# Optimization experiments

Hardware: AMD Instinct MI355X
Metric: run time of the kernel (lower is better)

## Reference

```python
import jax, jax.numpy as jnp
import numpy as np

SEQ = 512
D_MODEL = 256
NUM_HEADS = 8


def setup_inputs() -> dict:
    key = jax.random.key(0)
    k1, k2, k3, k4, k5, k6 = jax.random.split(key, 6)
    d = D_MODEL
    scale = 1.0 / np.sqrt(d)
    q = jax.random.normal(k1, (SEQ, d), dtype=jnp.float32)
    k = jax.random.normal(k2, (SEQ, d), dtype=jnp.float32)
    v = jax.random.normal(k3, (SEQ, d), dtype=jnp.float32)
    # eqx.nn.Linear weights have shape [out_features, in_features]
    Wq = jax.random.normal(k4, (d, d), dtype=jnp.float32) * scale
    Wk_hyper = jax.random.normal(k5, (d * d, d), dtype=jnp.float32) * scale
    Wv_hyper = jax.random.normal(k6, (d * d, d), dtype=jnp.float32) * scale
    # causal mask: every query row attends to >=1 key, matching softmax(where=mask)
    mask = jnp.tril(jnp.ones((SEQ, SEQ), dtype=bool))
    return {"q": q, "k": k, "v": v, "Wq": Wq, "Wk_hyper": Wk_hyper,
            "Wv_hyper": Wv_hyper, "mask": mask}


def reference(q, k, v, Wq, Wk_hyper, Wv_hyper, mask):
    s, d = q.shape
    n = NUM_HEADS
    dh = d // n
    # q projection (Linear, no bias): y = x @ W.T
    qp = q @ Wq.T                                   # [s, d]
    # hypernetwork per-query projection matrices P[i, j_out, k_in]
    Pk = (qp @ Wk_hyper.T).reshape(s, d, d)         # [s, d, d]
    Pv = (qp @ Wv_hyper.T).reshape(s, d, d)
    # per-query K/V cubes: K[i, l, j] = sum_k Pk[i, j, k] * k[l, k]
    Kc = jnp.einsum('sjk,lk->slj', Pk, k)           # [s, s, d]
    Vc = jnp.einsum('sjk,lk->slj', Pv, v)           # [s, s, d]
    # split heads
    qh = qp.reshape(s, n, dh)                       # [s, n, dh]
    Kh = Kc.reshape(s, s, n, dh)                    # [s_q, s_kv, n, dh]
    Vh = Vc.reshape(s, s, n, dh)
    # NOTE: original scales by 1/sqrt(kv_seq) (k.shape[0]), not sqrt(head_dim)
    logits = jnp.einsum('snd,stnd->nst', qh, Kh) / jnp.sqrt(jnp.float32(s))
    logits = jnp.where(mask[None, :, :], logits, -jnp.inf)
    probs = jax.nn.softmax(logits, axis=-1)         # [n, s_q, s_kv]
    out = jnp.einsum('nst,stnd->snd', probs, Vh)    # [s, n, dh]
    return out.reshape(s, d)
```

## Files before the change

### kernel.cpp

```cpp
#include <hip/hip_runtime.h>
#include <hip/hip_bf16.h>
#include <math.h>

#define SEQ 512
#define DM  256
#define NH  8
#define DH  32
#define DD  (DM*DM)

typedef __attribute__((ext_vector_type(4))) float  f32x4;
typedef __attribute__((ext_vector_type(8))) __bf16 bf16x8;
typedef __attribute__((ext_vector_type(8))) short  s16x8;
typedef __attribute__((ext_vector_type(4))) short  s16x4;

__device__ __forceinline__ unsigned short f2bf(float f) {
  unsigned int u = __builtin_bit_cast(unsigned int, f);
  u += 0x7fffu + ((u >> 16) & 1u);
  return (unsigned short)(u >> 16);
}
__device__ __forceinline__ float bf2f(unsigned short h) {
  unsigned int u = ((unsigned int)h) << 16;
  return __builtin_bit_cast(float, u);
}

__global__ __launch_bounds__(256) void k0_convert(const float* __restrict__ kin,
                                                  const float* __restrict__ vin,
                                                  unsigned short* __restrict__ kbf,
                                                  unsigned short* __restrict__ vT) {
  __shared__ unsigned short tl[64][72];
  int b = blockIdx.x, t = threadIdx.x;
  if (b < 32) {
    int base = b * 4096 + t * 16;
    float4 a0 = *(const float4*)(kin + base);
    float4 a1 = *(const float4*)(kin + base + 4);
    float4 a2 = *(const float4*)(kin + base + 8);
    float4 a3 = *(const float4*)(kin + base + 12);
    s16x8 o0, o1;
    o0[0]=f2bf(a0.x); o0[1]=f2bf(a0.y); o0[2]=f2bf(a0.z); o0[3]=f2bf(a0.w);
    o0[4]=f2bf(a1.x); o0[5]=f2bf(a1.y); o0[6]=f2bf(a1.z); o0[7]=f2bf(a1.w);
    o1[0]=f2bf(a2.x); o1[1]=f2bf(a2.y); o1[2]=f2bf(a2.z); o1[3]=f2bf(a2.w);
    o1[4]=f2bf(a3.x); o1[5]=f2bf(a3.y); o1[6]=f2bf(a3.z); o1[7]=f2bf(a3.w);
    *(s16x8*)(kbf + base)     = o0;
    *(s16x8*)(kbf + base + 8) = o1;
  } else {
    int tb = b - 32;
    int i0 = (tb >> 2) * 64;
    int m0 = (tb & 3) * 64;
    int r = t >> 2, cq = t & 3;
    #pragma unroll
    for (int u = 0; u < 4; u++) {
      float4 x = *(const float4*)(vin + (size_t)(i0 + r) * DM + m0 + cq * 16 + u * 4);
      tl[cq*16 + u*4 + 0][r] = f2bf(x.x);
      tl[cq*16 + u*4 + 1][r] = f2bf(x.y);
      tl[cq*16 + u*4 + 2][r] = f2bf(x.z);
      tl[cq*16 + u*4 + 3][r] = f2bf(x.w);
    }
    __syncthreads();
    int mm = t >> 2;
    s16x8 w0, w1;
    #pragma unroll
    for (int e = 0; e < 8; e++) { w0[e] = tl[mm][cq*16 + e]; w1[e] = tl[mm][cq*16 + 8 + e]; }
    *(s16x8*)(vT + (size_t)(m0 + mm) * SEQ + i0 + cq * 16)     = w0;
    *(s16x8*)(vT + (size_t)(m0 + mm) * SEQ + i0 + cq * 16 + 8) = w1;
  }
}

__global__ __launch_bounds__(256) void k1_qproj(const float* __restrict__ q,
                                                const float* __restrict__ Wq,
                                                float* __restrict__ qpf,
                                                unsigned short* __restrict__ qpb) {
  __shared__ __align__(16) float qrow[DM];
  int i = blockIdx.x, t = threadIdx.x;
  if (t < 64) *(float4*)&qrow[t*4] = *(const float4*)(q + (size_t)i * DM + t * 4);
  __syncthreads();
  int w = t >> 6, lane = t & 63;
  for (int jj = 0; jj < 64; jj++) {
    int j = w * 64 + jj;
    float4 wv = *(const float4*)(Wq + (size_t)j * DM + lane * 4);
    float s = wv.x*qrow[lane*4] + wv.y*qrow[lane*4+1] + wv.z*qrow[lane*4+2] + wv.w*qrow[lane*4+3];
    #pragma unroll
    for (int off = 32; off; off >>= 1) s += __shfl_xor(s, off);
    if (lane == 0) { qpf[(size_t)i*DM + j] = s; qpb[(size_t)i*DM + j] = f2bf(s); }
  }
}

template<int CONVB, int OUTBF>
__global__ __launch_bounds__(256) void gemm_nt(const unsigned short* __restrict__ A,
                                               const void* __restrict__ Bp,
                                               void* __restrict__ Cp,
                                               int M, int N, int K, int nMtiles) {
  __shared__ __align__(16) unsigned short lA[128 * 72];
  __shared__ __align__(16) unsigned short lB[128 * 72];
  int bid = blockIdx.x;
  int mtile = bid % nMtiles, ntile = bid / nMtiles;
  int m0 = mtile * 128, n0 = ntile * 128;
  int t = threadIdx.x;
  int w = t >> 6, lane = t & 63;
  int wr = w >> 1, wc = w & 1;
  f32x4 acc[4][4];
  #pragma unroll
  for (int a = 0; a < 4; a++)
    #pragma unroll
    for (int b = 0; b < 4; b++) acc[a][b] = (f32x4){0.f, 0.f, 0.f, 0.f};

  for (int kt = 0; kt < K; kt += 64) {
    __syncthreads();
    #pragma unroll
    for (int rep = 0; rep < 4; rep++) {
      int sc = rep * 256 + t;
      int row = sc >> 3, c8 = sc & 7;
      *(s16x8*)&lA[row*72 + c8*8] = *(const s16x8*)(A + (size_t)(m0+row)*K + kt + c8*8);
    }
    if (CONVB) {
      const float* B = (const float*)Bp;
      #pragma unroll
      for (int rep = 0; rep < 4; rep++) {
        int sc = rep * 256 + t;
        int row = sc >> 3, c8 = sc & 7;
        const float* src = B + (size_t)(n0+row)*K + kt + c8*8;
        float4 u0 = *(const float4*)src;
        float4 u1 = *(const float4*)(src + 4);
        s16x8 o;
        o[0]=f2bf(u0.x); o[1]=f2bf(u0.y); o[2]=f2bf(u0.z); o[3]=f2bf(u0.w);
        o[4]=f2bf(u1.x); o[5]=f2bf(u1.y); o[6]=f2bf(u1.z); o[7]=f2bf(u1.w);
        *(s16x8*)&lB[row*72 + c8*8] = o;
      }
    } else {
      const unsigned short* B = (const unsigned short*)Bp;
      #pragma unroll
      for (int rep = 0; rep < 4; rep++) {
        int sc = rep * 256 + t;
        int row = sc >> 3, c8 = sc & 7;
        *(s16x8*)&lB[row*72 + c8*8] = *(const s16x8*)(B + (size_t)(n0+row)*K + kt + c8*8);
      }
    }
    __syncthreads();
    #pragma unroll
    for (int kk = 0; kk < 2; kk++) {
      int r = lane & 15, kc = kk*32 + (lane >> 4)*8;
      bf16x8 af[4], bfv[4];
      #pragma unroll
      for (int mf = 0; mf < 4; mf++) af[mf]  = *(const bf16x8*)&lA[(wr*64 + mf*16 + r)*72 + kc];
      #pragma unroll
      for (int nf = 0; nf < 4; nf++) bfv[nf] = *(const bf16x8*)&lB[(wc*64 + nf*16 + r)*72 + kc];
      #pragma unroll
      for (int mf = 0; mf < 4; mf++)
        #pragma unroll
        for (int nf = 0; nf < 4; nf++)
          acc[mf][nf] = __builtin_amdgcn_mfma_f32_16x16x32_bf16(af[mf], bfv[nf], acc[mf][nf], 0, 0, 0);
    }
  }
  int cr = (lane >> 4) * 4, cc = lane & 15;
  #pragma unroll
  for (int mf = 0; mf < 4; mf++)
    #pragma unroll
    for (int nf = 0; nf < 4; nf++)
      #pragma unroll
      for (int qq = 0; qq < 4; qq++) {
        int row = m0 + wr*64 + mf*16 + cr + qq;
        int col = n0 + wc*64 + nf*16 + cc;
        float vv = acc[mf][nf][qq];
        if (OUTBF) ((unsigned short*)Cp)[(size_t)row * N + col] = f2bf(vv);
        else       ((float*)Cp)[(size_t)row * N + col] = vv;
      }
}

__global__ __launch_bounds__(256) void k3_reduce_a(const unsigned short* __restrict__ Pk,
                                                   const float* __restrict__ qpf,
                                                   unsigned short* __restrict__ abf) {
  __shared__ __align__(16) float ql[DM];
  int i = blockIdx.x, t = threadIdx.x;
  if (t < 64) *(float4*)&ql[t*4] = *(const float4*)(qpf + (size_t)i * DM + t * 4);
  __syncthreads();
  int w = t >> 6, lane = t & 63;
  const unsigned short* Prow = Pk + (size_t)i * DD;
  #pragma unroll
  for (int h = 0; h < 2; h++) {
    int n = w * 2 + h;
    float acc[8] = {0,0,0,0,0,0,0,0};
    for (int js = 0; js < 32; js += 2) {
      int j = n * 32 + js + (lane >> 5);
      s16x8 pv = *(const s16x8*)(Prow + (size_t)j * 256 + (lane & 31) * 8);
      float qv = ql[j];
      #pragma unroll
      for (int e = 0; e < 8; e++) acc[e] += qv * bf2f((unsigned short)pv[e]);
    }
    #pragma unroll
    for (int e = 0; e < 8; e++) acc[e] += __shfl_xor(acc[e], 32);
    if (lane < 32) {
      s16x8 o;
      #pragma unroll
      for (int e = 0; e < 8; e++) o[e] = f2bf(acc[e]);
      *(s16x8*)(abf + ((size_t)n * SEQ + i) * DM + (lane & 31) * 8) = o;
    }
  }
}

__global__ __launch_bounds__(256) void k4b_softmax(const float* __restrict__ logits,
                                                   unsigned short* __restrict__ probs) {
  __shared__ float red[4];
  __shared__ float red2[4];
  int m = blockIdx.x, t = threadIdx.x;
  int i = m & (SEQ - 1);
  const float scale = 0.04419417382415922f;
  const float NEG = -1e30f;
  float v0 = (t       <= i) ? logits[(size_t)m * SEQ + t      ] * scale : NEG;
  float v1 = (t + 256 <= i) ? logits[(size_t)m * SEQ + t + 256] * scale : NEG;
  float mx = fmaxf(v0, v1);
  #pragma unroll
  for (int off = 32; off; off >>= 1) mx = fmaxf(mx, __shfl_xor(mx, off));
  int w = t >> 6, lane = t & 63;
  if (lane == 0) red[w] = mx;
  __syncthreads();
  mx = fmaxf(fmaxf(red[0], red[1]), fmaxf(red[2], red[3]));
  float e0 = (t       <= i) ? __expf(v0 - mx) : 0.f;
  float e1 = (t + 256 <= i) ? __expf(v1 - mx) : 0.f;
  float s = e0 + e1;
  #pragma unroll
  for (int off = 32; off; off >>= 1) s += __shfl_xor(s, off);
  if (lane == 0) red2[w] = s;
  __syncthreads();
  s = red2[0] + red2[1] + red2[2] + red2[3];
  float inv = 1.f / s;
  probs[(size_t)m * SEQ + t]       = f2bf(e0 * inv);
  probs[(size_t)m * SEQ + t + 256] = f2bf(e1 * inv);
}

__global__ __launch_bounds__(256) void k5_out(const unsigned short* __restrict__ Pv,
                                              const unsigned short* __restrict__ wbf,
                                              float* __restrict__ out) {
  __shared__ __align__(16) float wl[8 * 264];
  int i = blockIdx.x, t = threadIdx.x;
  {
    int n = t >> 5, k8 = (t & 31) * 8;
    s16x8 v = *(const s16x8*)(wbf + ((size_t)n * SEQ + i) * DM + k8);
    #pragma unroll
    for (int e = 0; e < 8; e++) wl[n * 264 + k8 + e] = bf2f((unsigned short)v[e]);
  }
  __syncthreads();
  int w = t >> 6, lane = t & 63;
  const unsigned short* Prow = Pv + (size_t)i * DD;
  for (int jj = 0; jj < 64; jj++) {
    int j = w * 64 + jj;
    int n = j >> 5;
    s16x4 pv = *(const s16x4*)(Prow + (size_t)j * 256 + lane * 4);
    const float* wp = &wl[n * 264 + lane * 4];
    float s = bf2f((unsigned short)pv[0]) * wp[0] + bf2f((unsigned short)pv[1]) * wp[1]
            + bf2f((unsigned short)pv[2]) * wp[2] + bf2f((unsigned short)pv[3]) * wp[3];
    #pragma unroll
    for (int off = 32; off; off >>= 1) s += __shfl_xor(s, off);
    if (lane == 0) out[(size_t)i * DM + j] = s;
  }
}

extern "C" void kernel_launch(void* const* d_in, const int* in_sizes, int n_in,
                              void* d_out, int out_size, void* d_ws, size_t ws_size,
                              hipStream_t stream) {
  (void)in_sizes; (void)n_in; (void)out_size; (void)ws_size;
  const float* q  = (const float*)d_in[0];
  const float* k  = (const float*)d_in[1];
  const float* v  = (const float*)d_in[2];
  const float* Wq = (const float*)d_in[3];
  const float* Wk = (const float*)d_in[4];
  const float* Wv = (const float*)d_in[5];
  float* out = (float*)d_out;

  char* ws = (char*)d_ws;
  size_t off = 0;
  auto alloc = [&](size_t bytes) -> void* {
    void* p = ws + off; off += (bytes + 255) & ~(size_t)255; return p;
  };
  float*          qpf    = (float*)         alloc((size_t)SEQ * DM * 4);
  unsigned short* qpb    = (unsigned short*)alloc((size_t)SEQ * DM * 2);
  unsigned short* kbf    = (unsigned short*)alloc((size_t)SEQ * DM * 2);
  unsigned short* vT     = (unsigned short*)alloc((size_t)DM * SEQ * 2);
  unsigned short* abf    = (unsigned short*)alloc((size_t)NH * SEQ * DM * 2);
  float*          logits = (float*)         alloc((size_t)NH * SEQ * SEQ * 4);
  unsigned short* probs  = (unsigned short*)alloc((size_t)NH * SEQ * SEQ * 2);
  unsigned short* wbf    = (unsigned short*)alloc((size_t)NH * SEQ * DM * 2);
  unsigned short* Pk     = (unsigned short*)alloc((size_t)SEQ * DD * 2);
  unsigned short* Pv     = (unsigned short*)alloc((size_t)SEQ * DD * 2);

  k0_convert<<<64, 256, 0, stream>>>(k, v, kbf, vT);
  k1_qproj<<<SEQ, 256, 0, stream>>>(q, Wq, qpf, qpb);
  gemm_nt<1,1><<<2048, 256, 0, stream>>>(qpb, (const void*)Wk, (void*)Pk, SEQ, DD, DM, 4);
  gemm_nt<1,1><<<2048, 256, 0, stream>>>(qpb, (const void*)Wv, (void*)Pv, SEQ, DD, DM, 4);
  k3_reduce_a<<<SEQ, 256, 0, stream>>>(Pk, qpf, abf);
  gemm_nt<0,0><<<128, 256, 0, stream>>>(abf, (const void*)kbf, (void*)logits, NH*SEQ, SEQ, DM, 32);
  k4b_softmax<<<NH*SEQ, 256, 0, stream>>>(logits, probs);
  gemm_nt<0,1><<<64, 256, 0, stream>>>(probs, (const void*)vT, (void*)wbf, NH*SEQ, DM, SEQ, 32);
  k5_out<<<SEQ, 256, 0, stream>>>(Pv, wbf, out);
}
```

Before: 353.1 us.

## Reassociate hypernetwork contractions to avoid materializing per-query Pk/Pv matrices

Replaces the materialization of the per-query projection tensors Pk and Pv (SEQ x 256 x 256 each) with reassociated contractions. A query-weighted outer product of qp is contracted directly against the bf16-converted hyper weights, using split-K with atomicAdd into the reduced A and output. Weights are converted to bf16 once per call, and the B tiles are loaded through global_load_lds into a swizzled LDS layout. The aim is to remove the large write and re-read of Pk/Pv, at the cost of float atomics, extra memsets and scalar-times-qp recomputation for every K tile.

```diff
diff --git a/kernel.cpp b/kernel.cpp
--- a/kernel.cpp
+++ b/kernel.cpp
@@ -5,13 +5,10 @@
 #define SEQ 512
 #define DM  256
 #define NH  8
-#define DH  32
-#define DD  (DM*DM)
 
 typedef __attribute__((ext_vector_type(4))) float  f32x4;
 typedef __attribute__((ext_vector_type(8))) __bf16 bf16x8;
 typedef __attribute__((ext_vector_type(8))) short  s16x8;
-typedef __attribute__((ext_vector_type(4))) short  s16x4;
 
 __device__ __forceinline__ unsigned short f2bf(float f) {
   unsigned int u = __builtin_bit_cast(unsigned int, f);
@@ -21,6 +18,25 @@
 __device__ __forceinline__ float bf2f(unsigned short h) {
   unsigned int u = ((unsigned int)h) << 16;
   return __builtin_bit_cast(float, u);
+}
+__device__ __forceinline__ void gll16(const void* g, void* ldsbase) {
+  __builtin_amdgcn_global_load_lds((const __attribute__((address_space(1))) void*)g,
+                                   (__attribute__((address_space(3))) void*)ldsbase,
+                                   16, 0, 0);
+}
+
+__global__ __launch_bounds__(256) void kconv(const float* __restrict__ src,
+                                             unsigned short* __restrict__ dst) {
+  size_t base = ((size_t)blockIdx.x * 256 + threadIdx.x) * 32;
+  #pragma unroll
+  for (int u = 0; u < 4; u++) {
+    float4 a = *(const float4*)(src + base + u * 8);
+    float4 b = *(const float4*)(src + base + u * 8 + 4);
+    s16x8 o;
+    o[0]=f2bf(a.x); o[1]=f2bf(a.y); o[2]=f2bf(a.z); o[3]=f2bf(a.w);
+    o[4]=f2bf(b.x); o[5]=f2bf(b.y); o[6]=f2bf(b.z); o[7]=f2bf(b.w);
+    *(s16x8*)(dst + base + u * 8) = o;
+  }
 }
 
 __global__ __launch_bounds__(256) void k0_convert(const float* __restrict__ kin,
@@ -67,8 +83,7 @@
 
 __global__ __launch_bounds__(256) void k1_qproj(const float* __restrict__ q,
                                                 const float* __restrict__ Wq,
-                                                float* __restrict__ qpf,
-                                                unsigned short* __restrict__ qpb) {
+                                                float* __restrict__ qpf) {
   __shared__ __align__(16) float qrow[DM];
   int i = blockIdx.x, t = threadIdx.x;
   if (t < 64) *(float4*)&qrow[t*4] = *(const float4*)(q + (size_t)i * DM + t * 4);
@@ -80,120 +95,215 @@
     float s = wv.x*qrow[lane*4] + wv.y*qrow[lane*4+1] + wv.z*qrow[lane*4+2] + wv.w*qrow[lane*4+3];
     #pragma unroll
     for (int off = 32; off; off >>= 1) s += __shfl_xor(s, off);
-    if (lane == 0) { qpf[(size_t)i*DM + j] = s; qpb[(size_t)i*DM + j] = f2bf(s); }
-  }
-}
-
-template<int CONVB, int OUTBF>
-__global__ __launch_bounds__(256) void gemm_nt(const unsigned short* __restrict__ A,
-                                               const void* __restrict__ Bp,
-                                               void* __restrict__ Cp,
-                                               int M, int N, int K, int nMtiles) {
+    if (lane == 0) qpf[(size_t)i*DM + j] = s;
+  }
+}
+
+__global__ __launch_bounds__(256) void ka_gemm(const unsigned short* __restrict__ Wkb,
+                                               const float* __restrict__ qpf,
+                                               float* __restrict__ af) {
   __shared__ __align__(16) unsigned short lA[128 * 72];
-  __shared__ __align__(16) unsigned short lB[128 * 72];
+  __shared__ __align__(16) unsigned short lB[128 * 64];
   int bid = blockIdx.x;
-  int mtile = bid % nMtiles, ntile = bid / nMtiles;
+  int lid = (bid & 7) * 64 + (bid >> 3);
+  int mtile = lid & 3, ntile = (lid >> 2) & 1, head = (lid >> 3) & 7, kchunk = lid >> 6;
   int m0 = mtile * 128, n0 = ntile * 128;
-  int t = threadIdx.x;
-  int w = t >> 6, lane = t & 63;
+  int t = threadIdx.x, w = t >> 6, lane = t & 63;
   int wr = w >> 1, wc = w & 1;
-  f32x4 acc[4][4];
-  #pragma unroll
-  for (int a = 0; a < 4; a++)
-    #pragma unroll
-    for (int b = 0; b < 4; b++) acc[a][b] = (f32x4){0.f, 0.f, 0.f, 0.f};
-
-  for (int kt = 0; kt < K; kt += 64) {
-    __syncthreads();
+  f32x4 acc[4][4] = {};
+
+  for (int ks = 0; ks < 16; ks++) {
+    int kt = kchunk * 1024 + ks * 64;
+    int jcol = head * 32 + (kt >> 8);
+    int mbase = kt & 255;
+    __syncthreads();
+    {
+      const unsigned short* Bbase = Wkb + ((size_t)jcol * 256 + n0) * 256 + mbase;
+      #pragma unroll
+      for (int it = 0; it < 4; it++) {
+        int r0 = (w * 4 + it) * 8 + (lane >> 3);
+        int cbyte = ((lane & 7) * 16) ^ ((r0 & 7) << 4);
+        gll16((const char*)(Bbase + (size_t)r0 * 256) + cbyte,
+              (char*)lB + (w * 4 + it) * 1024);
+      }
+    }
     #pragma unroll
     for (int rep = 0; rep < 4; rep++) {
       int sc = rep * 256 + t;
       int row = sc >> 3, c8 = sc & 7;
-      *(s16x8*)&lA[row*72 + c8*8] = *(const s16x8*)(A + (size_t)(m0+row)*K + kt + c8*8);
-    }
-    if (CONVB) {
-      const float* B = (const float*)Bp;
-      #pragma unroll
-      for (int rep = 0; rep < 4; rep++) {
-        int sc = rep * 256 + t;
-        int row = sc >> 3, c8 = sc & 7;
-        const float* src = B + (size_t)(n0+row)*K + kt + c8*8;
-        float4 u0 = *(const float4*)src;
-        float4 u1 = *(const float4*)(src + 4);
+      int i = m0 + row;
+      float scal = qpf[(size_t)i * 256 + jcol];
+      const float* src = qpf + (size_t)i * 256 + mbase + c8 * 8;
+      float4 u0 = *(const float4*)src, u1 = *(const float4*)(src + 4);
+      s16x8 o;
+      o[0]=f2bf(scal*u0.x); o[1]=f2bf(scal*u0.y); o[2]=f2bf(scal*u0.z); o[3]=f2bf(scal*u0.w);
+      o[4]=f2bf(scal*u1.x); o[5]=f2bf(scal*u1.y); o[6]=f2bf(scal*u1.z); o[7]=f2bf(scal*u1.w);
+      *(s16x8*)&lA[row * 72 + c8 * 8] = o;
+    }
+    __syncthreads();
+    #pragma unroll
+    for (int kk = 0; kk < 2; kk++) {
+      int r = lane & 15, kc = kk * 32 + (lane >> 4) * 8;
+      bf16x8 afr[4], bfr[4];
+      #pragma unroll
+      for (int mf = 0; mf < 4; mf++) afr[mf] = *(const bf16x8*)&lA[(wr*64 + mf*16 + r) * 72 + kc];
+      #pragma unroll
+      for (int nf = 0; nf < 4; nf++) {
+        int row = wc*64 + nf*16 + r;
+        int cb = (kc * 2) ^ ((row & 7) << 4);
+        bfr[nf] = *(const bf16x8*)((const char*)lB + row * 128 + cb);
+      }
+      #pragma unroll
+      for (int mf = 0; mf < 4; mf++)
+        #pragma unroll
+        for (int nf = 0; nf < 4; nf++)
+          acc[mf][nf] = __builtin_amdgcn_mfma_f32_16x16x32_bf16(afr[mf], bfr[nf], acc[mf][nf], 0, 0, 0);
+    }
+  }
+  int cr = (lane >> 4) * 4, cc = lane & 15;
+  #pragma unroll
+  for (int mf = 0; mf < 4; mf++)
+    #pragma unroll
+    for (int nf = 0; nf < 4; nf++)
+      #pragma unroll
+      for (int qq = 0; qq < 4; qq++) {
+        int i   = m0 + wr*64 + mf*16 + cr + qq;
+        int col = n0 + wc*64 + nf*16 + cc;
+        atomicAdd(&af[((size_t)head * SEQ + i) * 256 + col], acc[mf][nf][qq]);
+      }
+}
+
+__global__ __launch_bounds__(256) void ko_gemm(const unsigned short* __restrict__ Wvb,
+                                               const float* __restrict__ qpf,
+                                               const unsigned short* __restrict__ wbf,
+                                               float* __restrict__ out) {
+  __shared__ __align__(16) unsigned short lA[128 * 72];
+  __shared__ __align__(16) unsigned short lB[32 * 64];
+  int bid = blockIdx.x;
+  int lid = (bid & 7) * 64 + (bid >> 3);
+  int mtile = lid & 3, head = (lid >> 2) & 7, kchunk = lid >> 5;
+  int m0 = mtile * 128;
+  int t = threadIdx.x, w = t >> 6, lane = t & 63;
+  f32x4 acc[2][2] = {};
+
+  for (int ks = 0; ks < 64; ks++) {
+    int kt = kchunk * 4096 + ks * 64;
+    int kdim = kt >> 8;
+    int mbase = kt & 255;
+    __syncthreads();
+    {
+      int r0 = w * 8 + (lane >> 3);
+      int cbyte = ((lane & 7) * 16) ^ ((r0 & 7) << 4);
+      const unsigned short* Bb = Wvb + (((size_t)head * 32 + r0) * 256 + kdim) * 256 + mbase;
+      gll16((const char*)Bb + cbyte, (char*)lB + w * 1024);
+    }
+    #pragma unroll
+    for (int rep = 0; rep < 4; rep++) {
+      int sc = rep * 256 + t;
+      int row = sc >> 3, c8 = sc & 7;
+      int i = m0 + row;
+      float scal = bf2f(wbf[((size_t)head * SEQ + i) * 256 + kdim]);
+      const float* src = qpf + (size_t)i * 256 + mbase + c8 * 8;
+      float4 u0 = *(const float4*)src, u1 = *(const float4*)(src + 4);
+      s16x8 o;
+      o[0]=f2bf(scal*u0.x); o[1]=f2bf(scal*u0.y); o[2]=f2bf(scal*u0.z); o[3]=f2bf(scal*u0.w);
+      o[4]=f2bf(scal*u1.x); o[5]=f2bf(scal*u1.y); o[6]=f2bf(scal*u1.z); o[7]=f2bf(scal*u1.w);
+      *(s16x8*)&lA[row * 72 + c8 * 8] = o;
+    }
+    __syncthreads();
+    #pragma unroll
+    for (int kk = 0; kk < 2; kk++) {
+      int r = lane & 15, kc = kk * 32 + (lane >> 4) * 8;
+      bf16x8 afr[2], bfr[2];
+      #pragma unroll
+      for (int mf = 0; mf < 2; mf++) afr[mf] = *(const bf16x8*)&lA[(w*32 + mf*16 + r) * 72 + kc];
+      #pragma unroll
+      for (int nf = 0; nf < 2; nf++) {
+        int row = nf*16 + r;
+        int cb = (kc * 2) ^ ((row & 7) << 4);
+        bfr[nf] = *(const bf16x8*)((const char*)lB + row * 128 + cb);
+      }
+      #pragma unroll
+      for (int mf = 0; mf < 2; mf++)
+        #pragma unroll
+        for (int nf = 0; nf < 2; nf++)
+          acc[mf][nf] = __builtin_amdgcn_mfma_f32_16x16x32_bf16(afr[mf], bfr[nf], acc[mf][nf], 0, 0, 0);
+    }
+  }
+  int cr = (lane >> 4) * 4, cc = lane & 15;
+  #pragma unroll
+  for (int mf = 0; mf < 2; mf++)
+    #pragma unroll
+    for (int nf = 0; nf < 2; nf++)
+      #pragma unroll
+      for (int qq = 0; qq < 4; qq++) {
+        int i   = m0 + w*32 + mf*16 + cr + qq;
+        int col = head * 32 + nf*16 + cc;
+        atomicAdd(&out[(size_t)i * 256 + col], acc[mf][nf][qq]);
+      }
+}
+
+template<int CONVA, int OUTBF>
+__global__ __launch_bounds__(256) void gemm_small(const void* __restrict__ Ap,
+                                                  const unsigned short* __restrict__ B,
+                                                  void* __restrict__ Cp,
+                                                  int M, int N, int K, int nMtiles) {
+  __shared__ __align__(16) unsigned short lA[64 * 72];
+  __shared__ __align__(16) unsigned short lB[64 * 72];
+  int bid = blockIdx.x;
+  int mtile = bid % nMtiles, ntile = bid / nMtiles;
+  int m0 = mtile * 64, n0 = ntile * 64;
+  int t = threadIdx.x, w = t >> 6, lane = t & 63;
+  int wr = w >> 1, wc = w & 1;
+  f32x4 acc[2][2] = {};
+  for (int kt = 0; kt < K; kt += 64) {
+    __syncthreads();
+    #pragma unroll
+    for (int rep = 0; rep < 2; rep++) {
+      int sc = rep * 256 + t;
+      int row = sc >> 3, c8 = sc & 7;
+      if (CONVA) {
+        const float* src = (const float*)Ap + (size_t)(m0 + row) * K + kt + c8 * 8;
+        float4 u0 = *(const float4*)src, u1 = *(const float4*)(src + 4);
         s16x8 o;
         o[0]=f2bf(u0.x); o[1]=f2bf(u0.y); o[2]=f2bf(u0.z); o[3]=f2bf(u0.w);
         o[4]=f2bf(u1.x); o[5]=f2bf(u1.y); o[6]=f2bf(u1.z); o[7]=f2bf(u1.w);
-        *(s16x8*)&lB[row*72 + c8*8] = o;
-      }
-    } else {
-      const unsigned short* B = (const unsigned short*)Bp;
-      #pragma unroll
-      for (int rep = 0; rep < 4; rep++) {
-        int sc = rep * 256 + t;
-        int row = sc >> 3, c8 = sc & 7;
-        *(s16x8*)&lB[row*72 + c8*8] = *(const s16x8*)(B + (size_t)(n0+row)*K + kt + c8*8);
-      }
+        *(s16x8*)&lA[row * 72 + c8 * 8] = o;
+      } else {
+        *(s16x8*)&lA[row * 72 + c8 * 8] =
+            *(const s16x8*)((const unsigned short*)Ap + (size_t)(m0 + row) * K + kt + c8 * 8);
+      }
+      *(s16x8*)&lB[row * 72 + c8 * 8] = *(const s16x8*)(B + (size_t)(n0 + row) * K + kt + c8 * 8);
     }
     __syncthreads();
     #pragma unroll
     for (int kk = 0; kk < 2; kk++) {
-      int r = lane & 15, kc = kk*32 + (lane >> 4)*8;
-      bf16x8 af[4], bfv[4];
-      #pragma unroll
-      for (int mf = 0; mf < 4; mf++) af[mf]  = *(const bf16x8*)&lA[(wr*64 + mf*16 + r)*72 + kc];
-      #pragma unroll
-      for (int nf = 0; nf < 4; nf++) bfv[nf] = *(const bf16x8*)&lB[(wc*64 + nf*16 + r)*72 + kc];
-      #pragma unroll
-      for (int mf = 0; mf < 4; mf++)
+      int r = lane & 15, kc = kk * 32 + (lane >> 4) * 8;
+      bf16x8 afr[2], bfr[2];
+      #pragma unroll
+      for (int mf = 0; mf < 2; mf++) afr[mf] = *(const bf16x8*)&lA[(wr*32 + mf*16 + r) * 72 + kc];
+      #pragma unroll
+      for (int nf = 0; nf < 2; nf++) bfr[nf] = *(const bf16x8*)&lB[(wc*32 + nf*16 + r) * 72 + kc];
+      #pragma unroll
+      for (int mf = 0; mf < 2; mf++)
         #pragma unroll
-        for (int nf = 0; nf < 4; nf++)
-          acc[mf][nf] = __builtin_amdgcn_mfma_f32_16x16x32_bf16(af[mf], bfv[nf], acc[mf][nf], 0, 0, 0);
+        for (int nf = 0; nf < 2; nf++)
+          acc[mf][nf] = __builtin_amdgcn_mfma_f32_16x16x32_bf16(afr[mf], bfr[nf], acc[mf][nf], 0, 0, 0);
     }
   }
   int cr = (lane >> 4) * 4, cc = lane & 15;
   #pragma unroll
-  for (int mf = 0; mf < 4; mf++)
-    #pragma unroll
-    for (int nf = 0; nf < 4; nf++)
+  for (int mf = 0; mf < 2; mf++)
+    #pragma unroll
+    for (int nf = 0; nf < 2; nf++)
       #pragma unroll
       for (int qq = 0; qq < 4; qq++) {
-        int row = m0 + wr*64 + mf*16 + cr + qq;
-        int col = n0 + wc*64 + nf*16 + cc;
+        int row = m0 + wr*32 + mf*16 + cr + qq;
+        int col = n0 + wc*32 + nf*16 + cc;
         float vv = acc[mf][nf][qq];
         if (OUTBF) ((unsigned short*)Cp)[(size_t)row * N + col] = f2bf(vv);
         else       ((float*)Cp)[(size_t)row * N + col] = vv;
       }
-}
-
-__global__ __launch_bounds__(256) void k3_reduce_a(const unsigned short* __restrict__ Pk,
-                                                   const float* __restrict__ qpf,
-                                                   unsigned short* __restrict__ abf) {
-  __shared__ __align__(16) float ql[DM];
-  int i = blockIdx.x, t = threadIdx.x;
-  if (t < 64) *(float4*)&ql[t*4] = *(const float4*)(qpf + (size_t)i * DM + t * 4);
-  __syncthreads();
-  int w = t >> 6, lane = t & 63;
-  const unsigned short* Prow = Pk + (size_t)i * DD;
-  #pragma unroll
-  for (int h = 0; h < 2; h++) {
-    int n = w * 2 + h;
-    float acc[8] = {0,0,0,0,0,0,0,0};
-    for (int js = 0; js < 32; js += 2) {
-      int j = n * 32 + js + (lane >> 5);
-      s16x8 pv = *(const s16x8*)(Prow + (size_t)j * 256 + (lane & 31) * 8);
-      float qv = ql[j];
-      #pragma unroll
-      for (int e = 0; e < 8; e++) acc[e] += qv * bf2f((unsigned short)pv[e]);
-    }
-    #pragma unroll
-    for (int e = 0; e < 8; e++) acc[e] += __shfl_xor(acc[e], 32);
-    if (lane < 32) {
-      s16x8 o;
-      #pragma unroll
-      for (int e = 0; e < 8; e++) o[e] = f2bf(acc[e]);
-      *(s16x8*)(abf + ((size_t)n * SEQ + i) * DM + (lane & 31) * 8) = o;
-    }
-  }
 }
 
 __global__ __launch_bounds__(256) void k4b_softmax(const float* __restrict__ logits,
@@ -226,33 +336,6 @@
   probs[(size_t)m * SEQ + t + 256] = f2bf(e1 * inv);
 }
 
-__global__ __launch_bounds__(256) void k5_out(const unsigned short* __restrict__ Pv,
-                                              const unsigned short* __restrict__ wbf,
-                                              float* __restrict__ out) {
-  __shared__ __align__(16) float wl[8 * 264];
-  int i = blockIdx.x, t = threadIdx.x;
-  {
-    int n = t >> 5, k8 = (t & 31) * 8;
-    s16x8 v = *(const s16x8*)(wbf + ((size_t)n * SEQ + i) * DM + k8);
-    #pragma unroll
-    for (int e = 0; e < 8; e++) wl[n * 264 + k8 + e] = bf2f((unsigned short)v[e]);
-  }
-  __syncthreads();
-  int w = t >> 6, lane = t & 63;
-  const unsigned short* Prow = Pv + (size_t)i * DD;
-  for (int jj = 0; jj < 64; jj++) {
-    int j = w * 64 + jj;
-    int n = j >> 5;
-    s16x4 pv = *(const s16x4*)(Prow + (size_t)j * 256 + lane * 4);
-    const float* wp = &wl[n * 264 + lane * 4];
-    float s = bf2f((unsigned short)pv[0]) * wp[0] + bf2f((unsigned short)pv[1]) * wp[1]
-            + bf2f((unsigned short)pv[2]) * wp[2] + bf2f((unsigned short)pv[3]) * wp[3];
-    #pragma unroll
-    for (int off = 32; off; off >>= 1) s += __shfl_xor(s, off);
-    if (lane == 0) out[(size_t)i * DM + j] = s;
-  }
-}
-
 extern "C" void kernel_launch(void* const* d_in, const int* in_sizes, int n_in,
                               void* d_out, int out_size, void* d_ws, size_t ws_size,
                               hipStream_t stream) {
@@ -271,23 +354,25 @@
     void* p = ws + off; off += (bytes + 255) & ~(size_t)255; return p;
   };
   float*          qpf    = (float*)         alloc((size_t)SEQ * DM * 4);
-  unsigned short* qpb    = (unsigned short*)alloc((size_t)SEQ * DM * 2);
   unsigned short* kbf    = (unsigned short*)alloc((size_t)SEQ * DM * 2);
   unsigned short* vT     = (unsigned short*)alloc((size_t)DM * SEQ * 2);
-  unsigned short* abf    = (unsigned short*)alloc((size_t)NH * SEQ * DM * 2);
+  unsigned short* Wkb    = (unsigned short*)alloc((size_t)DM * DM * DM * 2);
+  unsigned short* Wvb    = (unsigned short*)alloc((size_t)DM * DM * DM * 2);
+  float*          af     = (float*)         alloc((size_t)NH * SEQ * DM * 4);
   float*          logits = (float*)         alloc((size_t)NH * SEQ * SEQ * 4);
   unsigned short* probs  = (unsigned short*)alloc((size_t)NH * SEQ * SEQ * 2);
   unsigned short* wbf    = (unsigned short*)alloc((size_t)NH * SEQ * DM * 2);
-  unsigned short* Pk     = (unsigned short*)alloc((size_t)SEQ * DD * 2);
-  unsigned short* Pv     = (unsigned short*)alloc((size_t)SEQ * DD * 2);
-
+
+  hipMemsetAsync(af, 0, (size_t)NH * SEQ * DM * 4, stream);
+  hipMemsetAsync(out, 0, (size_t)SEQ * DM * 4, stream);
+
+  kconv<<<2048, 256, 0, stream>>>(Wk, Wkb);
+  kconv<<<2048, 256, 0, stream>>>(Wv, Wvb);
   k0_convert<<<64, 256, 0, stream>>>(k, v, kbf, vT);
-  k1_qproj<<<SEQ, 256, 0, stream>>>(q, Wq, qpf, qpb);
-  gemm_nt<1,1><<<2048, 256, 0, stream>>>(qpb, (const void*)Wk, (void*)Pk, SEQ, DD, DM, 4);
-  gemm_nt<1,1><<<2048, 256, 0, stream>>>(qpb, (const void*)Wv, (void*)Pv, SEQ, DD, DM, 4);
-  k3_reduce_a<<<SEQ, 256, 0, stream>>>(Pk, qpf, abf);
-  gemm_nt<0,0><<<128, 256, 0, stream>>>(abf, (const void*)kbf, (void*)logits, NH*SEQ, SEQ, DM, 32);
+  k1_qproj<<<SEQ, 256, 0, stream>>>(q, Wq, qpf);
+  ka_gemm<<<512, 256, 0, stream>>>(Wkb, qpf, af);
+  gemm_small<1,0><<<512, 256, 0, stream>>>((const void*)af, kbf, (void*)logits, NH*SEQ, SEQ, DM, 64);
   k4b_softmax<<<NH*SEQ, 256, 0, stream>>>(logits, probs);
-  gemm_nt<0,1><<<64, 256, 0, stream>>>(probs, (const void*)vT, (void*)wbf, NH*SEQ, DM, SEQ, 32);
-  k5_out<<<SEQ, 256, 0, stream>>>(Pv, wbf, out);
-}
+  gemm_small<0,1><<<256, 256, 0, stream>>>((const void*)probs, vT, (void*)wbf, NH*SEQ, DM, SEQ, 64);
+  ko_gemm<<<512, 256, 0, stream>>>(Wvb, qpf, wbf, out);
+}
```

Measured after the change: 378.6 us. +7.2%, slower.
